# Optimization experiments

Hardware: AMD Instinct MI355X
Metric: run time of the kernel (lower is better)

## Reference

```python
import jax, jax.numpy as jnp
import numpy as np

N = 100000      # nodes
E = 1600000     # edges per node-kind graph
H = 2           # attention heads
F_IN = 64
F_OUT = 64
N_USER = 90000
D2 = 64
NB_CLASSES = 2


def setup_inputs() -> dict:
    key = jax.random.key(0)
    ks = jax.random.split(key, 16)
    xav = lambda k, shape: jax.random.normal(k, shape, jnp.float32) * np.sqrt(2.0 / (shape[-2] + shape[-1]))
    inp = {
        "h": jax.random.normal(ks[0], (N, F_IN), jnp.float32),
        "src0": jax.random.randint(ks[1], (E,), 0, N, jnp.int32),
        "trg0": jax.random.randint(ks[2], (E,), 0, N, jnp.int32),
        "src1": jax.random.randint(ks[3], (E,), 0, N, jnp.int32),
        "trg1": jax.random.randint(ks[4], (E,), 0, N, jnp.int32),
        # SpGATLayer params per node kind
        "w0": xav(ks[5], (H, F_IN, F_OUT)),
        "asrc0": xav(ks[6], (H, F_OUT)),   # attn_src squeezed from (H, F_OUT, 1)
        "atrg0": xav(ks[7], (H, F_OUT)),
        "w1": xav(ks[8], (H, F_IN, F_OUT)),
        "asrc1": xav(ks[9], (H, F_OUT)),
        "atrg1": xav(ks[10], (H, F_OUT)),
        # AdditiveAttention params (nn.Linear weights: [out, in])
        "aa_w1": xav(ks[11], (D2, F_IN)),
        "aa_w2": xav(ks[12], (D2, F_OUT)),
        "aa_m": xav(ks[13], (1, D2)),
        # final fc: in = d1 * (nb_node_kinds + 1) = 64 * 3
        "fc_w": xav(ks[14], (NB_CLASSES, F_OUT * 3)),
        "fc_b": jnp.zeros((NB_CLASSES,), jnp.float32),
        "n_user": N_USER,
    }
    return inp


def sp_gat_layer(h, w, a_src, a_trg, src, trg, n):
    # h: [N, F_IN]; w: [H, F_IN, F_OUT]
    hp = jnp.einsum("nf,hfo->hno", h, w)                  # [H, N, F_OUT]
    attn_src = jnp.einsum("hno,ho->nh", hp, a_src)        # [N, H]
    attn_trg = jnp.einsum("hno,ho->nh", hp, a_trg)        # [N, H]
    e = jax.nn.leaky_relu(attn_src[src] + attn_trg[trg], 0.2)  # [E, H]
    e = e - jnp.max(e)                                    # global max, as in source
    exp_e = jnp.exp(e)
    denom = jax.ops.segment_sum(exp_e, trg, num_segments=n)[trg] + 1e-16
    attn = (exp_e / denom)[:, :, None]                    # [E, H, 1]
    hp_nhf = jnp.transpose(hp, (1, 0, 2))                 # [N, H, F_OUT]
    h_weighted = hp_nhf[src] * attn                       # [E, H, F_OUT]
    out = jax.ops.segment_sum(h_weighted, trg, num_segments=n)  # [N, H, F_OUT]
    return out


def reference(h, src0, trg0, src1, trg1, w0, asrc0, atrg0, w1, asrc1, atrg1,
              aa_w1, aa_w2, aa_m, fc_w, fc_b, n_user):
    n = h.shape[0]
    # one SpGAT layer per node kind, then mean over heads (final-layer branch)
    x0 = sp_gat_layer(h, w0, asrc0, atrg0, src0, trg0, n).mean(axis=1)  # [N, F_OUT]
    x1 = sp_gat_layer(h, w1, asrc1, atrg1, src1, trg1, n).mean(axis=1)
    type_aware = jnp.stack([x0[:n_user], x1[:n_user]], axis=1)          # [n_user, 2, F_OUT]
    # AdditiveAttention
    feat = h[:n_user]                                                   # [n_user, F_IN]
    q = jnp.tanh(feat @ aa_w1.T[:, None, :].squeeze(1)[None][0] if False else
                 jnp.tanh(0.0))  # placeholder removed below
    q = jnp.tanh(feat[:, None, :] @ aa_w1.T + type_aware @ aa_w2.T)     # [n_user, 2, D2]
    scores = (q @ aa_m.T).squeeze(-1)                                   # [n_user, 2]
    beta = jax.nn.softmax(scores, axis=-1)
    type_fusion = jnp.einsum("nk,nkd->nd", beta, type_aware)[:, None, :]  # [n_user, 1, F_OUT]
    cat = jnp.concatenate([type_aware, type_fusion], axis=1).reshape(n_user, -1)  # [n_user, 3*F_OUT]
    logits = cat @ fc_w.T + fc_b
    return jax.nn.log_softmax(logits, axis=-1)
```

## Files before the change

kernel.cpp:

```cpp
#include <hip/hip_runtime.h>
#include <hip/hip_bf16.h>
#include <math.h>

#define N_NODES 100000
#define N_EDGES 1600000
#define N_USER  90000
#define NBUCK   256
#define BSZ     352
#define TILE    2048
#define TBLK    782
#define ACCB    22500
#define HPB     1024

typedef __attribute__((ext_vector_type(8))) short  short8;
typedef __attribute__((ext_vector_type(4))) float  floatx4;
typedef unsigned int  uint;
typedef unsigned short ushort;

__device__ __forceinline__ ushort f2bf(float x) {
  uint u = __float_as_uint(x);
  u += 0x7fffu + ((u >> 16) & 1u);
  return (ushort)(u >> 16);
}
__device__ __forceinline__ float bf2f(ushort v) { return __uint_as_float(((uint)v) << 16); }

__device__ __forceinline__ void split8(const float v[8], short8& hi, short8& lo) {
  #pragma unroll
  for (int j = 0; j < 8; ++j) {
    ushort h = f2bf(v[j]);
    hi[j] = (short)h;
    lo[j] = (short)f2bf(v[j] - bf2f(h));
  }
}
__device__ __forceinline__ void load_split8(const float* p, short8& hi, short8& lo) {
  const float4* q = (const float4*)p;
  float4 a = q[0], b = q[1];
  float v[8] = {a.x, a.y, a.z, a.w, b.x, b.y, b.z, b.w};
  split8(v, hi, lo);
}
__device__ __forceinline__ float fast_tanh(float x) {
  float t = __expf(2.f * x);
  return 1.f - 2.f / (t + 1.f);
}

__global__ __launch_bounds__(256) void stage1(
    const float* __restrict__ h,
    const float* __restrict__ wA,  const float* __restrict__ wB,
    const float* __restrict__ asA, const float* __restrict__ asB,
    const float* __restrict__ atA, const float* __restrict__ atB,
    uint* __restrict__ hpiA, uint* __restrict__ hpiB,
    float* __restrict__ attnsA, float* __restrict__ attnsB,
    float* __restrict__ attntA, float* __restrict__ attntB,
    const int* __restrict__ trgA, const int* __restrict__ trgB,
    int* __restrict__ bhist,
    int hpTot, int hpBase, int bhBase)
{
  __shared__ float part[4][16][4];
  __shared__ int hh[NBUCK];
  const int tid = threadIdx.x;

  if (blockIdx.x >= hpTot) {
    const int b2 = blockIdx.x - hpTot;
    const int layer = (b2 >= bhBase) ? 1 : 0;
    const int bid = b2 - layer * bhBase;
    const int* trg = layer ? trgB : trgA;
    int* bh = bhist + layer * NBUCK;
    hh[tid] = 0;
    __syncthreads();
    const int b0 = bid * TILE;
    #pragma unroll
    for (int j = 0; j < 8; ++j) {
      int e = b0 + j * 256 + tid;
      if (e < N_EDGES) {
        int t = trg[e];
        if (t < N_USER) atomicAdd(&hh[t / BSZ], 1);
      }
    }
    __syncthreads();
    if (hh[tid]) atomicAdd(&bh[tid], hh[tid]);
    return;
  }

  const int layer = (blockIdx.x >= hpBase) ? 1 : 0;
  const int bid = blockIdx.x - layer * hpBase;
  const float* w     = layer ? wB : wA;
  const float* a_src = layer ? asB : asA;
  const float* a_trg = layer ? atB : atA;
  uint*  hpi      = layer ? hpiB : hpiA;
  float* attn_src = layer ? attnsB : attnsA;
  float* attn_trg = layer ? attntB : attntA;

  const int lane = tid & 63, wv = tid >> 6;
  const int quad = lane >> 4, l15 = lane & 15;
  const int o = wv * 16 + l15;
  const float vas0 = a_src[o], vas1 = a_src[64 + o];
  const float vat0 = a_trg[o], vat1 = a_trg[64 + o];
  short8 b0h[2], b0l[2], b1h[2], b1l[2];
  #pragma unroll
  for (int ks = 0; ks < 2; ++ks) {
    float v0[8], v1[8];
    #pragma unroll
    for (int j = 0; j < 8; ++j) {
      int k = quad * 8 + j + ks * 32;
      v0[j] = w[k * 64 + o];
      v1[j] = w[4096 + k * 64 + o];
    }
    split8(v0, b0h[ks], b0l[ks]);
    split8(v1, b1h[ks], b1l[ks]);
  }
  for (int t = bid; t < N_NODES / 16; t += hpBase) {
    int m0 = t * 16, arow = m0 + l15;
    short8 ah[2], al[2];
    #pragma unroll
    for (int ks = 0; ks < 2; ++ks)
      load_split8(h + arow * 64 + quad * 8 + ks * 32, ah[ks], al[ks]);
    floatx4 c0 = {0.f, 0.f, 0.f, 0.f}, c1 = {0.f, 0.f, 0.f, 0.f};
    #pragma unroll
    for (int ks = 0; ks < 2; ++ks) {
      c0 = __builtin_amdgcn_mfma_f32_16x16x32_bf16(ah[ks], b0h[ks], c0, 0, 0, 0);
      c0 = __builtin_amdgcn_mfma_f32_16x16x32_bf16(ah[ks], b0l[ks], c0, 0, 0, 0);
      c0 = __builtin_amdgcn_mfma_f32_16x16x32_bf16(al[ks], b0h[ks], c0, 0, 0, 0);
      c1 = __builtin_amdgcn_mfma_f32_16x16x32_bf16(ah[ks], b1h[ks], c1, 0, 0, 0);
      c1 = __builtin_amdgcn_mfma_f32_16x16x32_bf16(ah[ks], b1l[ks], c1, 0, 0, 0);
      c1 = __builtin_amdgcn_mfma_f32_16x16x32_bf16(al[ks], b1h[ks], c1, 0, 0, 0);
    }
    #pragma unroll
    for (int r = 0; r < 4; ++r) {
      int n = m0 + quad * 4 + r;
      hpi[n * 64 + o] = (uint)f2bf(c0[r]) | ((uint)f2bf(c1[r]) << 16);
    }
    #pragma unroll
    for (int r = 0; r < 4; ++r) {
      float pas0 = c0[r] * vas0, pas1 = c1[r] * vas1;
      float pat0 = c0[r] * vat0, pat1 = c1[r] * vat1;
      #pragma unroll
      for (int m = 1; m < 16; m <<= 1) {
        pas0 += __shfl_xor(pas0, m, 64); pas1 += __shfl_xor(pas1, m, 64);
        pat0 += __shfl_xor(pat0, m, 64); pat1 += __shfl_xor(pat1, m, 64);
      }
      if (l15 == 0) {
        part[wv][quad * 4 + r][0] = pas0; part[wv][quad * 4 + r][1] = pas1;
        part[wv][quad * 4 + r][2] = pat0; part[wv][quad * 4 + r][3] = pat1;
      }
    }
    __syncthreads();
    if (tid < 64) {
      int row = tid & 15, which = tid >> 4;
      float v = part[0][row][which] + part[1][row][which]
              + part[2][row][which] + part[3][row][which];
      int n = m0 + row;
      if (which == 0)      attn_src[n * 2]     = v;
      else if (which == 1) attn_src[n * 2 + 1] = v;
      else if (which == 2) attn_trg[n * 2]     = v;
      else                 attn_trg[n * 2 + 1] = v;
    }
    __syncthreads();
  }
}

__global__ __launch_bounds__(256) void scanb2(const int* __restrict__ bhist,
                                              int* __restrict__ bstart, int* __restrict__ bcur)
{
  const int layer = blockIdx.x;
  const int* bh = bhist + layer * NBUCK;
  int* bs = bstart + layer * (NBUCK + 1);
  int* bc = bcur + layer * NBUCK * 16;
  __shared__ int s[256];
  int v = bh[threadIdx.x];
  s[threadIdx.x] = v;
  __syncthreads();
  for (int d = 1; d < 256; d <<= 1) {
    int t = (threadIdx.x >= d) ? s[threadIdx.x - d] : 0;
    __syncthreads();
    s[threadIdx.x] += t;
    __syncthreads();
  }
  int excl = s[threadIdx.x] - v;
  bs[threadIdx.x] = excl;
  bc[threadIdx.x * 16] = excl;
  if (threadIdx.x == 255) bs[256] = s[255];
}

__global__ __launch_bounds__(256) void bucket2(
    const int* __restrict__ srcA, const int* __restrict__ srcB,
    const int* __restrict__ trgA, const int* __restrict__ trgB,
    int* __restrict__ bcur, uint* __restrict__ pairbufA, uint* __restrict__ pairbufB, int base)
{
  const int layer = (blockIdx.x >= base) ? 1 : 0;
  const int bid = blockIdx.x - layer * base;
  const int* src = layer ? srcB : srcA;
  const int* trg = layer ? trgB : trgA;
  int* bc = bcur + layer * NBUCK * 16;
  uint* pairbuf = layer ? pairbufB : pairbufA;

  __shared__ uint2 plds[TILE];
  __shared__ int bcnt[NBUCK], bscan[NBUCK], gbase[NBUCK];
  const int tid = threadIdx.x;
  const int b0 = bid * TILE;
  bcnt[tid] = 0;
  __syncthreads();
  int myb[8], myr[8];
  uint myp[8];
  #pragma unroll
  for (int j = 0; j < 8; ++j) {
    int e = b0 + j * 256 + tid;
    myb[j] = -1;
    if (e < N_EDGES) {
      int t = trg[e];
      if (t < N_USER) {
        int b = t / BSZ;
        int tl = t - b * BSZ;
        myb[j] = b;
        myr[j] = atomicAdd(&bcnt[b], 1);
        myp[j] = (uint)src[e] | ((uint)tl << 17);
      }
    }
  }
  __syncthreads();
  gbase[tid] = atomicAdd(&bc[tid * 16], bcnt[tid]);
  bscan[tid] = bcnt[tid];
  __syncthreads();
  for (int d = 1; d < 256; d <<= 1) {
    int v = (tid >= d) ? bscan[tid - d] : 0;
    __syncthreads();
    bscan[tid] += v;
    __syncthreads();
  }
  #pragma unroll
  for (int j = 0; j < 8; ++j)
    if (myb[j] >= 0) plds[bscan[myb[j]] - bcnt[myb[j]] + myr[j]] = make_uint2(myp[j], (uint)myb[j]);
  __syncthreads();
  int total = bscan[NBUCK - 1];
  for (int i = tid; i < total; i += 256) {
    uint2 pr = plds[i];
    int b = (int)pr.y;
    int idx = gbase[b] + (i - (bscan[b] - bcnt[b]));
    if (idx >= 0 && idx < N_EDGES) pairbuf[idx] = pr.x;
  }
}

__global__ __launch_bounds__(1024) void fine2(
    const uint* __restrict__ pairbufA, const uint* __restrict__ pairbufB,
    const int* __restrict__ bstart,
    int* __restrict__ offsA, int* __restrict__ offsB,
    int* __restrict__ csrA,  int* __restrict__ csrB,
    const float* __restrict__ attnsA, const float* __restrict__ attnsB,
    const float* __restrict__ attntA, const float* __restrict__ attntB,
    float2* __restrict__ wgtA, float2* __restrict__ wgtB, int base)
{
  const int layer = (blockIdx.x >= base) ? 1 : 0;
  const int b = blockIdx.x - layer * base;
  const uint* pairbuf = layer ? pairbufB : pairbufA;
  const int* bs = bstart + layer * (NBUCK + 1);
  int* offs = layer ? offsB : offsA;
  int* csr_src = layer ? csrB : csrA;
  const float* attn_src = layer ? attnsB : attnsA;
  const float* attn_trg = layer ? attntB : attntA;
  float2* wgt = layer ? wgtB : wgtA;

  __shared__ int cnt[BSZ + 1];
  __shared__ int cur[BSZ];
  const int tid = threadIdx.x;
  const int t0 = b * BSZ;
  const int nt = min(BSZ, N_USER - t0);
  const int pbeg = bs[b], pend = bs[b + 1];
  for (int j = tid; j <= BSZ; j += 1024) cnt[j] = 0;
  __syncthreads();
  for (int i = pbeg + tid; i < pend; i += 1024) {
    int tl = min((int)(pairbuf[i] >> 17), BSZ - 1);
    atomicAdd(&cnt[tl], 1);
  }
  __syncthreads();
  if (tid == 0) {
    int run = 0;
    for (int j = 0; j < nt; ++j) { int c = cnt[j]; cnt[j] = run; run += c; }
    cnt[nt] = run;
  }
  __syncthreads();
  for (int j = tid; j < nt; j += 1024) {
    offs[t0 + j] = pbeg + cnt[j];
    cur[j] = cnt[j];
  }
  if (tid == 0 && t0 + nt == N_USER) offs[N_USER] = pbeg + cnt[nt];
  __syncthreads();
  const float2* as2 = (const float2*)attn_src;
  const float2* at2 = (const float2*)attn_trg;
  for (int i = pbeg + tid; i < pend; i += 1024) {
    uint v = pairbuf[i];
    int s = min((int)(v & 0x1FFFFu), N_NODES - 1);
    int tl = min((int)(v >> 17), BSZ - 1);
    int tt = min(t0 + tl, N_USER - 1);
    float2 as = as2[s];
    float2 at = at2[tt];
    float e0 = as.x + at.x; e0 = (e0 > 0.f) ? e0 : 0.2f * e0;
    float e1 = as.y + at.y; e1 = (e1 > 0.f) ? e1 : 0.2f * e1;
    int p = pbeg + atomicAdd(&cur[tl], 1);
    p = min(max(p, 0), N_EDGES - 1);
    csr_src[p] = s;
    wgt[p] = make_float2(__expf(e0), __expf(e1));
  }
}

__global__ __launch_bounds__(256) void accum2(
    const int* __restrict__ offsA, const int* __restrict__ offsB,
    const int* __restrict__ csrA,  const int* __restrict__ csrB,
    const float2* __restrict__ wgtA, const float2* __restrict__ wgtB,
    const uint* __restrict__ hpiA, const uint* __restrict__ hpiB,
    float* __restrict__ xA, float* __restrict__ xB, int base, int swz)
{
  int layer, bid;
  if (swz) {
    const int xcd = blockIdx.x & 7, idx = blockIdx.x >> 3;
    layer = xcd >> 2;
    bid = idx * 4 + (xcd & 3);
  } else {
    layer = (blockIdx.x >= base) ? 1 : 0;
    bid = blockIdx.x - layer * base;
  }
  const int* offs = layer ? offsB : offsA;
  const int* csr_src = layer ? csrB : csrA;
  const float2* wgt = layer ? wgtB : wgtA;
  const uint* hpi = layer ? hpiB : hpiA;
  float* x = layer ? xB : xA;

  const int lane = threadIdx.x & 63, wv = threadIdx.x >> 6;
  int n = bid * 4 + wv;
  if (n >= N_USER) return;
  int beg = max(0, offs[n]);
  int end = min(offs[n + 1], N_EDGES);
  beg = __builtin_amdgcn_readfirstlane(beg);
  end = __builtin_amdgcn_readfirstlane(end);
  int deg = end - beg;
  float acc0 = 0.f, acc1 = 0.f, den0 = 0.f, den1 = 0.f;
  for (int base2 = 0; base2 < deg; base2 += 64) {
    int rem = min(64, deg - base2);
    int sv = csr_src[beg + base2 + min(lane, rem - 1)];
    sv = min(max(sv, 0), N_NODES - 1);
    int nfull = rem & ~7;
    for (int j = 0; j < nfull; j += 8) {
      int ss[8]; uint pv[8]; float2 W[8];
      #pragma unroll
      for (int u = 0; u < 8; ++u) ss[u] = __builtin_amdgcn_readlane(sv, j + u);
      #pragma unroll
      for (int u = 0; u < 8; ++u) pv[u] = (hpi + (size_t)ss[u] * 64)[lane];
      #pragma unroll
      for (int u = 0; u < 8; ++u) W[u] = wgt[beg + base2 + j + u];
      #pragma unroll
      for (int u = 0; u < 8; ++u) {
        den0 += W[u].x; den1 += W[u].y;
        acc0 += W[u].x * bf2f((ushort)(pv[u] & 0xffffu));
        acc1 += W[u].y * bf2f((ushort)(pv[u] >> 16));
      }
    }
    if (nfull < rem) {
      int j = nfull;
      int ss[8]; uint pv[8]; float2 W[8];
      #pragma unroll
      for (int u = 0; u < 8; ++u) ss[u] = __builtin_amdgcn_readlane(sv, min(j + u, rem - 1));
      #pragma unroll
      for (int u = 0; u < 8; ++u) pv[u] = (hpi + (size_t)ss[u] * 64)[lane];
      #pragma unroll
      for (int u = 0; u < 8; ++u)
        W[u] = (j + u < rem) ? wgt[beg + base2 + j + u] : make_float2(0.f, 0.f);
      #pragma unroll
      for (int u = 0; u < 8; ++u) {
        den0 += W[u].x; den1 += W[u].y;
        acc0 += W[u].x * bf2f((ushort)(pv[u] & 0xffffu));
        acc1 += W[u].y * bf2f((ushort)(pv[u] >> 16));
      }
    }
  }
  x[n * 64 + lane] = 0.5f * (acc0 / (den0 + 1e-16f) + acc1 / (den1 + 1e-16f));
}

__global__ __launch_bounds__(256) void final_mfma(
    const float* __restrict__ h, const float* __restrict__ x0, const float* __restrict__ x1,
    const float* __restrict__ aa_w1, const float* __restrict__ aa_w2, const float* __restrict__ aa_m,
    const float* __restrict__ fc_w, const float* __restrict__ fc_b, float* __restrict__ out)
{
  __shared__ float aam_s[64], fcw_s[384], fcb_s[2];
  __shared__ float scw0[2][4][16], scw1[2][4][16];
  const int tid = threadIdx.x;
  if (tid < 64)  aam_s[tid] = aa_m[tid];
  for (int i = tid; i < 384; i += 256) fcw_s[i] = fc_w[i];
  if (tid < 2)   fcb_s[tid] = fc_b[tid];
  const int lane = tid & 63, wv = tid >> 6, quad = lane >> 4, l15 = lane & 15;
  const int d = wv * 16 + l15;
  short8 b1h[2], b1l[2], b2h[2], b2l[2];
  #pragma unroll
  for (int ks = 0; ks < 2; ++ks) {
    load_split8(aa_w1 + d * 64 + quad * 8 + ks * 32, b1h[ks], b1l[ks]);
    load_split8(aa_w2 + d * 64 + quad * 8 + ks * 32, b2h[ks], b2l[ks]);
  }
  __syncthreads();
  int pp = 0;
  for (int t = blockIdx.x; t < N_USER / 16; t += gridDim.x) {
    int m0 = t * 16, arow = m0 + l15;
    const int erow = m0 + wv * 4 + quad;
    float4 ev0 = *(const float4*)(x0 + erow * 64 + l15 * 4);
    float4 ev1 = *(const float4*)(x1 + erow * 64 + l15 * 4);
    short8 ahh[2], ahl[2], a0h[2], a0l[2], a1h[2], a1l[2];
    #pragma unroll
    for (int ks = 0; ks < 2; ++ks) {
      load_split8(h  + arow * 64 + quad * 8 + ks * 32, ahh[ks], ahl[ks]);
      load_split8(x0 + arow * 64 + quad * 8 + ks * 32, a0h[ks], a0l[ks]);
      load_split8(x1 + arow * 64 + quad * 8 + ks * 32, a1h[ks], a1l[ks]);
    }
    floatx4 t1a = {0.f,0.f,0.f,0.f}, t20a = {0.f,0.f,0.f,0.f}, t21a = {0.f,0.f,0.f,0.f};
    #pragma unroll
    for (int ks = 0; ks < 2; ++ks) {
      t1a  = __builtin_amdgcn_mfma_f32_16x16x32_bf16(ahh[ks], b1h[ks], t1a, 0, 0, 0);
      t1a  = __builtin_amdgcn_mfma_f32_16x16x32_bf16(ahh[ks], b1l[ks], t1a, 0, 0, 0);
      t1a  = __builtin_amdgcn_mfma_f32_16x16x32_bf16(ahl[ks], b1h[ks], t1a, 0, 0, 0);
      t20a = __builtin_amdgcn_mfma_f32_16x16x32_bf16(a0h[ks], b2h[ks], t20a, 0, 0, 0);
      t20a = __builtin_amdgcn_mfma_f32_16x16x32_bf16(a0h[ks], b2l[ks], t20a, 0, 0, 0);
      t20a = __builtin_amdgcn_mfma_f32_16x16x32_bf16(a0l[ks], b2h[ks], t20a, 0, 0, 0);
      t21a = __builtin_amdgcn_mfma_f32_16x16x32_bf16(a1h[ks], b2h[ks], t21a, 0, 0, 0);
      t21a = __builtin_amdgcn_mfma_f32_16x16x32_bf16(a1h[ks], b2l[ks], t21a, 0, 0, 0);
      t21a = __builtin_amdgcn_mfma_f32_16x16x32_bf16(a1l[ks], b2h[ks], t21a, 0, 0, 0);
    }
    float am = aam_s[d];
    #pragma unroll
    for (int r = 0; r < 4; ++r) {
      float q0 = fast_tanh(t1a[r] + t20a[r]);
      float q1 = fast_tanh(t1a[r] + t21a[r]);
      float p0 = q0 * am, p1 = q1 * am;
      #pragma unroll
      for (int m = 1; m < 16; m <<= 1) { p0 += __shfl_xor(p0, m, 64); p1 += __shfl_xor(p1, m, 64); }
      if (l15 == 0) { scw0[pp][wv][quad * 4 + r] = p0; scw1[pp][wv][quad * 4 + r] = p1; }
    }
    __syncthreads();
    {
      int row = wv * 4 + quad, n = m0 + row;
      float s0 = scw0[pp][0][row] + scw0[pp][1][row] + scw0[pp][2][row] + scw0[pp][3][row];
      float s1 = scw1[pp][0][row] + scw1[pp][1][row] + scw1[pp][2][row] + scw1[pp][3][row];
      float mx = fmaxf(s0, s1);
      float e0 = __expf(s0 - mx), e1 = __expf(s1 - mx);
      float inv = 1.f / (e0 + e1);
      float b0 = e0 * inv, b1 = e1 * inv;
      float a0[4] = {ev0.x, ev0.y, ev0.z, ev0.w};
      float a1[4] = {ev1.x, ev1.y, ev1.z, ev1.w};
      float pc0 = 0.f, pc1 = 0.f;
      #pragma unroll
      for (int c = 0; c < 4; ++c) {
        int o = l15 * 4 + c;
        float fv = b0 * a0[c] + b1 * a1[c];
        pc0 += fcw_s[o] * a0[c] + fcw_s[64 + o] * a1[c] + fcw_s[128 + o] * fv;
        pc1 += fcw_s[192 + o] * a0[c] + fcw_s[256 + o] * a1[c] + fcw_s[320 + o] * fv;
      }
      #pragma unroll
      for (int m = 1; m < 16; m <<= 1) { pc0 += __shfl_xor(pc0, m, 64); pc1 += __shfl_xor(pc1, m, 64); }
      if (l15 == 0) {
        float l0 = pc0 + fcb_s[0], l1 = pc1 + fcb_s[1];
        float lm = fmaxf(l0, l1);
        float lse = lm + logf(__expf(l0 - lm) + __expf(l1 - lm));
        out[n * 2] = l0 - lse;
        out[n * 2 + 1] = l1 - lse;
      }
    }
    pp ^= 1;
  }
}

extern "C" void kernel_launch(void* const* d_in, const int* in_sizes, int n_in,
                              void* d_out, int out_size, void* d_ws, size_t ws_size,
                              hipStream_t stream)
{
  const float* h     = (const float*)d_in[0];
  const int*   src0  = (const int*)d_in[1];
  const int*   trg0  = (const int*)d_in[2];
  const int*   src1  = (const int*)d_in[3];
  const int*   trg1  = (const int*)d_in[4];
  const float* w0    = (const float*)d_in[5];
  const float* asrc0 = (const float*)d_in[6];
  const float* atrg0 = (const float*)d_in[7];
  const float* w1    = (const float*)d_in[8];
  const float* asrc1 = (const float*)d_in[9];
  const float* atrg1 = (const float*)d_in[10];
  const float* aa_w1 = (const float*)d_in[11];
  const float* aa_w2 = (const float*)d_in[12];
  const float* aa_m  = (const float*)d_in[13];
  const float* fc_w  = (const float*)d_in[14];
  const float* fc_b  = (const float*)d_in[15];
  float* out = (float*)d_out;

  const int nl = (ws_size >= (size_t)162 * 1024 * 1024) ? 2 : 1;
  const size_t L = (size_t)(nl - 1);

  char* ws = (char*)d_ws;
  size_t off = 0;
  auto alloc = [&](size_t bytes) -> void* {
    void* p = ws + off;
    off = (off + bytes + 255) & ~(size_t)255;
    return p;
  };
  uint*   hpi      = (uint*)alloc((size_t)nl * N_NODES * 64 * 4);
  float*  attn_src = (float*)alloc((size_t)nl * N_NODES * 2 * 4);
  float*  attn_trg = (float*)alloc((size_t)nl * N_NODES * 2 * 4);
  float*  x0       = (float*)alloc((size_t)N_USER * 64 * 4);
  float*  x1       = (float*)alloc((size_t)N_USER * 64 * 4);
  int*    offs     = (int*)alloc((size_t)nl * (N_USER + 1) * 4);
  int*    csr      = (int*)alloc((size_t)nl * N_EDGES * 4);
  uint*   pairbuf  = (uint*)alloc((size_t)nl * N_EDGES * 4);
  float2* wgt      = (float2*)alloc((size_t)nl * N_EDGES * 8);
  int*    bhist    = (int*)alloc((size_t)2 * NBUCK * 4);
  int*    bstart   = (int*)alloc((size_t)2 * (NBUCK + 1) * 4);
  int*    bcur     = (int*)alloc((size_t)2 * NBUCK * 16 * 4);

  uint*   hpi1     = hpi + L * (size_t)N_NODES * 64;
  float*  attns1   = attn_src + L * (size_t)N_NODES * 2;
  float*  attnt1   = attn_trg + L * (size_t)N_NODES * 2;
  int*    offs1    = offs + L * (size_t)(N_USER + 1);
  int*    csr1     = csr + L * (size_t)N_EDGES;
  uint*   pairbuf1 = pairbuf + L * (size_t)N_EDGES;
  float2* wgt1     = wgt + L * (size_t)N_EDGES;

  if (nl == 2) {
    hipMemsetAsync(bhist, 0, (size_t)2 * NBUCK * 4, stream);
    hipLaunchKernelGGL(stage1, dim3(2 * HPB + 2 * TBLK), dim3(256), 0, stream,
                       h, w0, w1, asrc0, asrc1, atrg0, atrg1,
                       hpi, hpi1, attn_src, attns1, attn_trg, attnt1,
                       trg0, trg1, bhist, 2 * HPB, HPB, TBLK);
    hipLaunchKernelGGL(scanb2, dim3(2), dim3(256), 0, stream, bhist, bstart, bcur);
    hipLaunchKernelGGL(bucket2, dim3(2 * TBLK), dim3(256), 0, stream,
                       src0, src1, trg0, trg1, bcur, pairbuf, pairbuf1, TBLK);
    hipLaunchKernelGGL(fine2, dim3(2 * NBUCK), dim3(1024), 0, stream,
                       pairbuf, pairbuf1, bstart, offs, offs1, csr, csr1,
                       attn_src, attns1, attn_trg, attnt1, wgt, wgt1, NBUCK);
    hipLaunchKernelGGL(accum2, dim3(2 * ACCB), dim3(256), 0, stream,
                       offs, offs1, csr, csr1, wgt, wgt1, hpi, hpi1, x0, x1, ACCB, 1);
  } else {
    for (int layer = 0; layer < 2; ++layer) {
      const float* w    = layer ? w1 : w0;
      const float* asrc = layer ? asrc1 : asrc0;
      const float* atrg = layer ? atrg1 : atrg0;
      const int*   src  = layer ? src1 : src0;
      const int*   trg  = layer ? trg1 : trg0;
      float*       x    = layer ? x1 : x0;
      hipMemsetAsync(bhist, 0, (size_t)NBUCK * 4, stream);
      hipLaunchKernelGGL(stage1, dim3(HPB + TBLK), dim3(256), 0, stream,
                         h, w, w, asrc, asrc, atrg, atrg,
                         hpi, hpi, attn_src, attn_src, attn_trg, attn_trg,
                         trg, trg, bhist, HPB, HPB, TBLK);
      hipLaunchKernelGGL(scanb2, dim3(1), dim3(256), 0, stream, bhist, bstart, bcur);
      hipLaunchKernelGGL(bucket2, dim3(TBLK), dim3(256), 0, stream,
                         src, src, trg, trg, bcur, pairbuf, pairbuf, TBLK);
      hipLaunchKernelGGL(fine2, dim3(NBUCK), dim3(1024), 0, stream,
                         pairbuf, pairbuf, bstart, offs, offs, csr, csr,
                         attn_src, attn_src, attn_trg, attn_trg, wgt, wgt, NBUCK);
      hipLaunchKernelGGL(accum2, dim3(ACCB), dim3(256), 0, stream,
                         offs, offs, csr, csr, wgt, wgt, hpi, hpi, x, x, ACCB, 0);
    }
  }
  hipLaunchKernelGGL(final_mfma, dim3(1875), dim3(256), 0, stream,
                     h, x0, x1, aa_w1, aa_w2, aa_m, fc_w, fc_b, out);
}
```

Before: 426.0 us.

## Fuse edge aggregation with additive-attention and classifier epilogue

Replaces the separate accum2 aggregation and final_mfma kernels with one kernel per 16 user nodes. Each block gathers both layers' neighbour features into shared memory, then runs the attention MLP with MFMA and the FC/log-softmax in place. This removes the x0/x1 global round trip and one launch. In exchange it changes the work split and the XCD swizzle: one wave now handles 4 nodes serially per layer instead of the accum2 layout, which may lower parallelism for the gather phase.

```diff
diff --git a/kernel.cpp b/kernel.cpp
--- a/kernel.cpp
+++ b/kernel.cpp
@@ -298,6 +298,156 @@
     p = min(max(p, 0), N_EDGES - 1);
     csr_src[p] = s;
     wgt[p] = make_float2(__expf(e0), __expf(e1));
+  }
+}
+
+__global__ __launch_bounds__(256) void accfin(
+    const int* __restrict__ offs0, const int* __restrict__ offs1,
+    const int* __restrict__ csr0,  const int* __restrict__ csr1,
+    const float2* __restrict__ wgt0, const float2* __restrict__ wgt1,
+    const uint* __restrict__ hpi0, const uint* __restrict__ hpi1,
+    const float* __restrict__ h,
+    const float* __restrict__ aa_w1, const float* __restrict__ aa_w2,
+    const float* __restrict__ aa_m,
+    const float* __restrict__ fc_w, const float* __restrict__ fc_b,
+    float* __restrict__ out)
+{
+  __shared__ float xs[2][16][68];
+  __shared__ float aam_s[64], fcw_s[384], fcb_s[2];
+  __shared__ float scw0[4][16], scw1[4][16];
+  const int tid = threadIdx.x;
+  const int lane = tid & 63, wv = tid >> 6, quad = lane >> 4, l15 = lane & 15;
+  const int m0 = blockIdx.x * 16;
+  if (tid < 64)  aam_s[tid] = aa_m[tid];
+  for (int i = tid; i < 384; i += 256) fcw_s[i] = fc_w[i];
+  if (tid < 2)   fcb_s[tid] = fc_b[tid];
+
+  #pragma unroll
+  for (int li = 0; li < 2; ++li) {
+    const int* offs = li ? offs1 : offs0;
+    const int* csr_src = li ? csr1 : csr0;
+    const float2* wgt = li ? wgt1 : wgt0;
+    const uint* hpi = li ? hpi1 : hpi0;
+    for (int k = 0; k < 4; ++k) {
+      int n = m0 + wv * 4 + k;
+      int beg = max(0, offs[n]);
+      int end = min(offs[n + 1], N_EDGES);
+      beg = __builtin_amdgcn_readfirstlane(beg);
+      end = __builtin_amdgcn_readfirstlane(end);
+      int deg = end - beg;
+      float acc0 = 0.f, acc1 = 0.f, den0 = 0.f, den1 = 0.f;
+      for (int base2 = 0; base2 < deg; base2 += 64) {
+        int rem = min(64, deg - base2);
+        int sv = csr_src[beg + base2 + min(lane, rem - 1)];
+        sv = min(max(sv, 0), N_NODES - 1);
+        int nfull = rem & ~7;
+        for (int j = 0; j < nfull; j += 8) {
+          int ss[8]; uint pv[8]; float2 W[8];
+          #pragma unroll
+          for (int u = 0; u < 8; ++u) ss[u] = __builtin_amdgcn_readlane(sv, j + u);
+          #pragma unroll
+          for (int u = 0; u < 8; ++u) pv[u] = (hpi + (size_t)ss[u] * 64)[lane];
+          #pragma unroll
+          for (int u = 0; u < 8; ++u) W[u] = wgt[beg + base2 + j + u];
+          #pragma unroll
+          for (int u = 0; u < 8; ++u) {
+            den0 += W[u].x; den1 += W[u].y;
+            acc0 += W[u].x * bf2f((ushort)(pv[u] & 0xffffu));
+            acc1 += W[u].y * bf2f((ushort)(pv[u] >> 16));
+          }
+        }
+        if (nfull < rem) {
+          int j = nfull;
+          int ss[8]; uint pv[8]; float2 W[8];
+          #pragma unroll
+          for (int u = 0; u < 8; ++u) ss[u] = __builtin_amdgcn_readlane(sv, min(j + u, rem - 1));
+          #pragma unroll
+          for (int u = 0; u < 8; ++u) pv[u] = (hpi + (size_t)ss[u] * 64)[lane];
+          #pragma unroll
+          for (int u = 0; u < 8; ++u)
+            W[u] = (j + u < rem) ? wgt[beg + base2 + j + u] : make_float2(0.f, 0.f);
+          #pragma unroll
+          for (int u = 0; u < 8; ++u) {
+            den0 += W[u].x; den1 += W[u].y;
+            acc0 += W[u].x * bf2f((ushort)(pv[u] & 0xffffu));
+            acc1 += W[u].y * bf2f((ushort)(pv[u] >> 16));
+          }
+        }
+      }
+      xs[li][wv * 4 + k][lane] = 0.5f * (acc0 / (den0 + 1e-16f) + acc1 / (den1 + 1e-16f));
+    }
+  }
+  __syncthreads();
+
+  const int d = wv * 16 + l15;
+  short8 b1h[2], b1l[2], b2h[2], b2l[2];
+  #pragma unroll
+  for (int ks = 0; ks < 2; ++ks) {
+    load_split8(aa_w1 + d * 64 + quad * 8 + ks * 32, b1h[ks], b1l[ks]);
+    load_split8(aa_w2 + d * 64 + quad * 8 + ks * 32, b2h[ks], b2l[ks]);
+  }
+  const int arow = m0 + l15;
+  const int erw = wv * 4 + quad;
+  float4 ev0 = *(const float4*)&xs[0][erw][l15 * 4];
+  float4 ev1 = *(const float4*)&xs[1][erw][l15 * 4];
+  short8 ahh[2], ahl[2], a0h[2], a0l[2], a1h[2], a1l[2];
+  #pragma unroll
+  for (int ks = 0; ks < 2; ++ks) {
+    load_split8(h + arow * 64 + quad * 8 + ks * 32, ahh[ks], ahl[ks]);
+    load_split8(&xs[0][l15][quad * 8 + ks * 32], a0h[ks], a0l[ks]);
+    load_split8(&xs[1][l15][quad * 8 + ks * 32], a1h[ks], a1l[ks]);
+  }
+  floatx4 t1a = {0.f,0.f,0.f,0.f}, t20a = {0.f,0.f,0.f,0.f}, t21a = {0.f,0.f,0.f,0.f};
+  #pragma unroll
+  for (int ks = 0; ks < 2; ++ks) {
+    t1a  = __builtin_amdgcn_mfma_f32_16x16x32_bf16(ahh[ks], b1h[ks], t1a, 0, 0, 0);
+    t1a  = __builtin_amdgcn_mfma_f32_16x16x32_bf16(ahh[ks], b1l[ks], t1a, 0, 0, 0);
+    t1a  = __builtin_amdgcn_mfma_f32_16x16x32_bf16(ahl[ks], b1h[ks], t1a, 0, 0, 0);
+    t20a = __builtin_amdgcn_mfma_f32_16x16x32_bf16(a0h[ks], b2h[ks], t20a, 0, 0, 0);
+    t20a = __builtin_amdgcn_mfma_f32_16x16x32_bf16(a0h[ks], b2l[ks], t20a, 0, 0, 0);
+    t20a = __builtin_amdgcn_mfma_f32_16x16x32_bf16(a0l[ks], b2h[ks], t20a, 0, 0, 0);
+    t21a = __builtin_amdgcn_mfma_f32_16x16x32_bf16(a1h[ks], b2h[ks], t21a, 0, 0, 0);
+    t21a = __builtin_amdgcn_mfma_f32_16x16x32_bf16(a1h[ks], b2l[ks], t21a, 0, 0, 0);
+    t21a = __builtin_amdgcn_mfma_f32_16x16x32_bf16(a1l[ks], b2h[ks], t21a, 0, 0, 0);
+  }
+  float am = aam_s[d];
+  #pragma unroll
+  for (int r = 0; r < 4; ++r) {
+    float q0 = fast_tanh(t1a[r] + t20a[r]);
+    float q1 = fast_tanh(t1a[r] + t21a[r]);
+    float p0 = q0 * am, p1 = q1 * am;
+    #pragma unroll
+    for (int m = 1; m < 16; m <<= 1) { p0 += __shfl_xor(p0, m, 64); p1 += __shfl_xor(p1, m, 64); }
+    if (l15 == 0) { scw0[wv][quad * 4 + r] = p0; scw1[wv][quad * 4 + r] = p1; }
+  }
+  __syncthreads();
+  {
+    int row = wv * 4 + quad, n = m0 + row;
+    float s0 = scw0[0][row] + scw0[1][row] + scw0[2][row] + scw0[3][row];
+    float s1 = scw1[0][row] + scw1[1][row] + scw1[2][row] + scw1[3][row];
+    float mx = fmaxf(s0, s1);
+    float e0 = __expf(s0 - mx), e1 = __expf(s1 - mx);
+    float inv = 1.f / (e0 + e1);
+    float b0 = e0 * inv, b1 = e1 * inv;
+    float a0[4] = {ev0.x, ev0.y, ev0.z, ev0.w};
+    float a1[4] = {ev1.x, ev1.y, ev1.z, ev1.w};
+    float pc0 = 0.f, pc1 = 0.f;
+    #pragma unroll
+    for (int c = 0; c < 4; ++c) {
+      int o = l15 * 4 + c;
+      float fv = b0 * a0[c] + b1 * a1[c];
+      pc0 += fcw_s[o] * a0[c] + fcw_s[64 + o] * a1[c] + fcw_s[128 + o] * fv;
+      pc1 += fcw_s[192 + o] * a0[c] + fcw_s[256 + o] * a1[c] + fcw_s[320 + o] * fv;
+    }
+    #pragma unroll
+    for (int m = 1; m < 16; m <<= 1) { pc0 += __shfl_xor(pc0, m, 64); pc1 += __shfl_xor(pc1, m, 64); }
+    if (l15 == 0) {
+      float l0 = pc0 + fcb_s[0], l1 = pc1 + fcb_s[1];
+      float lm = fmaxf(l0, l1);
+      float lse = lm + logf(__expf(l0 - lm) + __expf(l1 - lm));
+      out[n * 2] = l0 - lse;
+      out[n * 2 + 1] = l1 - lse;
+    }
   }
 }
 
@@ -527,8 +677,9 @@
     hipLaunchKernelGGL(fine2, dim3(2 * NBUCK), dim3(1024), 0, stream,
                        pairbuf, pairbuf1, bstart, offs, offs1, csr, csr1,
                        attn_src, attns1, attn_trg, attnt1, wgt, wgt1, NBUCK);
-    hipLaunchKernelGGL(accum2, dim3(2 * ACCB), dim3(256), 0, stream,
-                       offs, offs1, csr, csr1, wgt, wgt1, hpi, hpi1, x0, x1, ACCB, 1);
+    hipLaunchKernelGGL(accfin, dim3(N_USER / 16), dim3(256), 0, stream,
+                       offs, offs1, csr, csr1, wgt, wgt1, hpi, hpi1,
+                       h, aa_w1, aa_w2, aa_m, fc_w, fc_b, out);
   } else {
     for (int layer = 0; layer < 2; ++layer) {
       const float* w    = layer ? w1 : w0;
@@ -551,7 +702,7 @@
       hipLaunchKernelGGL(accum2, dim3(ACCB), dim3(256), 0, stream,
                          offs, offs, csr, csr, wgt, wgt, hpi, hpi, x, x, ACCB, 0);
     }
-  }
-  hipLaunchKernelGGL(final_mfma, dim3(1875), dim3(256), 0, stream,
-                     h, x0, x1, aa_w1, aa_w2, aa_m, fc_w, fc_b, out);
-}
+    hipLaunchKernelGGL(final_mfma, dim3(1875), dim3(256), 0, stream,
+                       h, x0, x1, aa_w1, aa_w2, aa_m, fc_w, fc_b, out);
+  }
+}
```

New measurement: 430.6 us. Within noise of the previous version (+1.1%).
